# Optimization experiments

Hardware: AMD Instinct MI355X
Metric: run time of the kernel (lower is better)

Reference implementation:

```python
import jax, jax.numpy as jnp
from jax import lax
import numpy as np

N_LOOP, N_LAYER, FS = 2, 10, 2
RES_CH, DIL_CH, SKIP_CH, COND_DIM = 64, 128, 128, 80
DILATIONS = [2 ** i for i in range(N_LAYER)] * N_LOOP  # 20 layers
L = len(DILATIONS)
B, T = 4, 8192


def setup_inputs() -> dict:
    key = jax.random.key(0)
    ks = jax.random.split(key, 10)
    s = 0.05
    return {
        "x": jax.random.normal(ks[0], (B, RES_CH, T, 1), jnp.float32),
        "condition": jax.random.normal(ks[1], (B, COND_DIM, T, 1), jnp.float32),
        # stacked per-layer params (L layers)
        "conv_w": jax.random.normal(ks[2], (L, DIL_CH, RES_CH, FS), jnp.float32) * s,
        "conv_b": jax.random.normal(ks[3], (L, DIL_CH), jnp.float32) * s,
        "cond_w": jax.random.normal(ks[4], (L, DIL_CH, COND_DIM), jnp.float32) * s,
        "cond_b": jax.random.normal(ks[5], (L, DIL_CH), jnp.float32) * s,
        "res_w": jax.random.normal(ks[6], (L, RES_CH, DIL_CH // 2), jnp.float32) * s,
        "res_b": jax.random.normal(ks[7], (L, RES_CH), jnp.float32) * s,
        "skip_w": jax.random.normal(ks[8], (L, SKIP_CH, DIL_CH // 2), jnp.float32) * s,
        "skip_b": jax.random.normal(ks[9], (L, SKIP_CH), jnp.float32) * s,
    }


def reference(x, condition, conv_w, conv_b, cond_w, cond_b, res_w, res_b, skip_w, skip_b):
    # Drop trailing width-1 dim: [B,C,T,1] -> [B,C,T]
    xs = x[..., 0]
    cond = condition[..., 0]
    skip_total = None
    for i, d in enumerate(DILATIONS):
        # torch pads d*(FS-1) on both sides then crops [:T] == left-only causal pad
        h = lax.conv_general_dilated(
            xs, conv_w[i], window_strides=(1,),
            padding=[(d * (FS - 1), 0)], rhs_dilation=(d,),
            dimension_numbers=("NCH", "OIH", "NCH"),
        ) + conv_b[i][None, :, None]
        # 1x1 condition projection, broadcast add
        h = h + jnp.einsum("ch,bht->bct", cond_w[i], cond) + cond_b[i][None, :, None]
        tanh_z, sig_z = jnp.split(h, 2, axis=1)
        z = jnp.tanh(tanh_z) * jax.nn.sigmoid(sig_z)  # [B, DIL_CH//2, T]
        xs = jnp.einsum("oc,bct->bot", res_w[i], z) + res_b[i][None, :, None] + xs
        skip = jnp.einsum("oc,bct->bot", skip_w[i], z) + skip_b[i][None, :, None]
        skip_total = skip if skip_total is None else skip_total + skip
    return skip_total[..., None]  # [B, SKIP_CH, T, 1]
```

## Files before the change

kernel.cpp:

```cpp
#include <hip/hip_runtime.h>

#define BATCH 4
#define TLEN 8192
#define NLAYER 20
#define NTILE 128
#define GUARD 8
#define ATILE (NTILE + GUARD)
#define CELL 4096

typedef __attribute__((ext_vector_type(8))) short bf16x8;
typedef __attribute__((ext_vector_type(8))) unsigned short u16x8;
typedef __attribute__((ext_vector_type(4))) short s16x4;
typedef __attribute__((ext_vector_type(4))) float f32x4;

__device__ __forceinline__ unsigned short f2b(float f) {
    unsigned u = __float_as_uint(f);
    return (unsigned short)((u + 0x7fffu + ((u >> 16) & 1u)) >> 16);
}

__global__ void prep_w(const float* __restrict__ conv_w, const float* __restrict__ conv_b,
                       const float* __restrict__ cond_w, const float* __restrict__ cond_b,
                       const float* __restrict__ res_w,  const float* __restrict__ res_b,
                       const float* __restrict__ skip_w, const float* __restrict__ skip_b,
                       unsigned short* __restrict__ w1f, unsigned short* __restrict__ w2f,
                       unsigned short* __restrict__ wsf,
                       float* __restrict__ hb, float* __restrict__ rb, float* __restrict__ sbt) {
    const int l = blockIdx.x, tid = threadIdx.x;
    const int start = blockIdx.y * 256 + tid;
    for (int idx = start; idx < 7 * 8 * 512; idx += 2048) {
        int ks = idx >> 12;
        int lane = (idx >> 3) & 63, j = idx & 7, mf = (idx >> 9) & 7;
        int m = mf * 16 + (lane & 15);
        int k = ks * 32 + ((lane >> 4) << 3) + j;
        float v;
        if (k < 64)       v = conv_w[(((size_t)l * 128 + m) * 64 + k) * 2 + 0];
        else if (k < 128) v = conv_w[(((size_t)l * 128 + m) * 64 + (k - 64)) * 2 + 1];
        else if (k < 208) v = cond_w[((size_t)l * 128 + m) * 80 + (k - 128)];
        else              v = 0.0f;
        w1f[(size_t)l * 7 * 8 * 512 + idx] = f2b(v);
    }
    for (int idx = start; idx < 2 * 4 * 512; idx += 2048) {
        int ks = idx >> 11;
        int slot = (idx >> 9) & 3, lane = (idx >> 3) & 63, j = idx & 7;
        int m = slot * 16 + (lane & 15);
        int k = ks * 32 + ((lane >> 4) << 3) + j;
        w2f[(size_t)l * 2 * 4 * 512 + idx] = f2b(res_w[((size_t)l * 64 + m) * 64 + k]);
    }
    for (int idx = start; idx < 2 * 8 * 512; idx += 2048) {
        int ks = idx >> 12;
        int slot = (idx >> 9) & 7, lane = (idx >> 3) & 63, j = idx & 7;
        int m = slot * 16 + (lane & 15);
        int k = ks * 32 + ((lane >> 4) << 3) + j;
        wsf[(size_t)l * 2 * 8 * 512 + idx] = f2b(skip_w[((size_t)l * 128 + m) * 64 + k]);
    }
    if (blockIdx.y == 0) {
        if (tid < 128) hb[l * 128 + tid] = conv_b[l * 128 + tid] + cond_b[l * 128 + tid];
        if (tid < 64)  rb[l * 64 + tid] = res_b[l * 64 + tid];
        if (l == 0 && tid < 128) {
            float s = 0.f;
            for (int q = 0; q < NLAYER; ++q) s += skip_b[q * 128 + tid];
            sbt[tid] = s;
        }
    }
}

__global__ void prep_cond(const float* __restrict__ cond, unsigned short* __restrict__ condc) {
    __shared__ float ct[80][64];
    const int tile = blockIdx.x, b = blockIdx.y, tid = threadIdx.x;
    for (int idx = tid; idx < 80 * 64; idx += 256) {
        int ch = idx >> 6, n = idx & 63;
        ct[ch][n] = cond[((size_t)b * 80 + ch) * TLEN + tile * 64 + n];
    }
    __syncthreads();
    for (int idx = tid; idx < 12 * 64; idx += 256) {
        int cg = idx >> 6, n = idx & 63;
        u16x8 cell;
        #pragma unroll
        for (int j = 0; j < 8; ++j) {
            int ch = cg * 8 + j;
            cell[j] = (ch < 80) ? f2b(ct[ch][n]) : (unsigned short)0;
        }
        *(u16x8*)(condc + (((size_t)(b * NTILE + tile) * 12 + cg) * 64 + n) * 8) = cell;
    }
}

__global__ void prep_x(const float* __restrict__ x, unsigned short* __restrict__ xall,
                       unsigned* __restrict__ flags) {
    const int tile = blockIdx.x, b = blockIdx.y, tid = threadIdx.x;
    if (tile < GUARD) {
        s16x4 zh = {0, 0, 0, 0};
        for (int s = 0; s < NLAYER; ++s) {
            unsigned short* g = xall + ((size_t)s * BATCH + b) * ATILE * CELL + (size_t)tile * CELL;
            for (int idx = tid * 4; idx < CELL; idx += 1024)
                *(s16x4*)(g + idx) = zh;
        }
        if (tile == 0)
            for (int i = tid; i < NTILE * 32; i += 256)
                flags[(size_t)b * NTILE * 32 + i] = 0u;
        return;
    }
    __shared__ float xt[64][64];
    const int rt = tile - GUARD;
    for (int idx = tid; idx < 64 * 64; idx += 256) {
        int ch = idx >> 6, n = idx & 63;
        xt[ch][n] = x[((size_t)b * 64 + ch) * TLEN + rt * 64 + n];
    }
    __syncthreads();
    unsigned short* s0 = xall + ((size_t)b * ATILE + tile) * CELL;
    for (int idx = tid; idx < 8 * 64; idx += 256) {
        int cg = idx >> 6, n = idx & 63;
        unsigned short* dbf = s0 + ((size_t)cg * 64 + n) * 8;
        #pragma unroll
        for (int j = 0; j < 8; ++j) dbf[j] = f2b(xt[cg * 8 + j][n]);
    }
}

__global__ __launch_bounds__(256, 2) void wavenet_fused(
    const float* __restrict__ x, const unsigned short* __restrict__ condc,
    unsigned short* __restrict__ xall,
    const unsigned short* __restrict__ w1f, const unsigned short* __restrict__ w2f,
    const unsigned short* __restrict__ wsf,
    const float* __restrict__ hb, const float* __restrict__ rb,
    const float* __restrict__ sbt, float* __restrict__ out,
    unsigned* __restrict__ flags) {
    __shared__ unsigned short s_cond[12 * 512];
    __shared__ unsigned short s_xc[CELL];
    __shared__ unsigned short s_zc[CELL];
    __shared__ float H[128][67];

    const int b = blockIdx.y, tile = blockIdx.x, t0 = tile * 64;
    const int tid = threadIdx.x, lane = tid & 63;
    const int wv = __builtin_amdgcn_readfirstlane(tid >> 6);
    const int ln = lane & 15, lg = lane >> 4;
    const int r0 = wv * 16 + lg * 4;
    const size_t bslot = (size_t)BATCH * ATILE * CELL;

    {
        const u16x8* cc = (const u16x8*)(condc + (size_t)(b * NTILE + tile) * 12 * 512);
        u16x8* sc = (u16x8*)s_cond;
        for (int i = tid; i < 768; i += 256) sc[i] = cc[i];
        const u16x8* xc = (const u16x8*)(xall + ((size_t)b * ATILE + tile + GUARD) * CELL);
        u16x8* sx = (u16x8*)s_xc;
        for (int i = tid; i < 512; i += 256) sx[i] = xc[i];
    }

    f32x4 xsr[4];
    #pragma unroll
    for (int nf = 0; nf < 4; ++nf)
        #pragma unroll
        for (int r = 0; r < 4; ++r)
            xsr[nf][r] = x[((size_t)b * 64 + r0 + r) * TLEN + t0 + nf * 16 + ln];

    f32x4 skacc[2][4];
    #pragma unroll
    for (int mf = 0; mf < 2; ++mf)
        #pragma unroll
        for (int nf = 0; nf < 4; ++nf) skacc[mf][nf] = (f32x4){0.f, 0.f, 0.f, 0.f};

    __syncthreads();

    for (int l = 0; l < NLAYER; ++l) {
        const int dil = 1 << ((l < 10) ? l : (l - 10));

        if (l > 0) {
            if (tid == 0) {
                int tp = tile - ((dil + 63) >> 6);
                if (tp >= 0) {
                    const unsigned* fp = flags + ((size_t)b * NTILE + tp) * 32;
                    while (__hip_atomic_load(fp, __ATOMIC_RELAXED, __HIP_MEMORY_SCOPE_AGENT) < (unsigned)l)
                        __builtin_amdgcn_s_sleep(2);
                }
            }
            __syncthreads();
        }

        const unsigned short* xrb = xall + (size_t)l * bslot + (size_t)b * ATILE * CELL;

        f32x4 acc[2][4];
        #pragma unroll
        for (int mf = 0; mf < 2; ++mf)
            #pragma unroll
            for (int nf = 0; nf < 4; ++nf) acc[mf][nf] = (f32x4){0.f, 0.f, 0.f, 0.f};

        const unsigned short* w1l = w1f + (size_t)l * 7 * 8 * 512;
        #pragma unroll
        for (int ks = 0; ks < 7; ++ks) {
            bf16x8 af0 = *(const bf16x8*)(w1l + (size_t)(ks * 8 + wv * 2 + 0) * 512 + lane * 8);
            bf16x8 af1 = *(const bf16x8*)(w1l + (size_t)(ks * 8 + wv * 2 + 1) * 512 + lane * 8);
            bf16x8 bfr[4];
            if (ks < 2) {
                const int cg = ks * 4 + lg;
                #pragma unroll
                for (int nf = 0; nf < 4; ++nf) {
                    int u = t0 + nf * 16 + ln - dil + GUARD * 64;
                    bfr[nf] = *(const bf16x8*)(xrb + (((size_t)(u >> 6) * 8 + cg) * 64 + (u & 63)) * 8);
                }
            } else if (ks < 4) {
                const int cg = (ks - 2) * 4 + lg;
                #pragma unroll
                for (int nf = 0; nf < 4; ++nf)
                    bfr[nf] = *(const bf16x8*)(s_xc + ((cg * 64) + nf * 16 + ln) * 8);
            } else {
                const int cg = (ks - 4) * 4 + lg;
                #pragma unroll
                for (int nf = 0; nf < 4; ++nf)
                    bfr[nf] = *(const bf16x8*)(s_cond + ((cg * 64) + nf * 16 + ln) * 8);
            }
            #pragma unroll
            for (int mf = 0; mf < 2; ++mf)
                #pragma unroll
                for (int nf = 0; nf < 4; ++nf)
                    acc[mf][nf] = __builtin_amdgcn_mfma_f32_16x16x32_bf16(
                        (mf == 0) ? af0 : af1, bfr[nf], acc[mf][nf], 0, 0, 0);
        }

        const float* hbl = hb + l * 128;
        #pragma unroll
        for (int mf = 0; mf < 2; ++mf)
            #pragma unroll
            for (int nf = 0; nf < 4; ++nf)
                #pragma unroll
                for (int r = 0; r < 4; ++r) {
                    int m = wv * 32 + mf * 16 + lg * 4 + r;
                    H[m][nf * 16 + ln] = acc[mf][nf][r] + hbl[m];
                }
        __syncthreads();

        {
            const int n = tid & 63, g0 = (tid >> 6) * 16;
            #pragma unroll
            for (int half = 0; half < 2; ++half) {
                const int rbase = g0 + half * 8;
                u16x8 cell;
                #pragma unroll
                for (int i = 0; i < 4; ++i) {
                    int r = rbase + 2 * i;
                    float a0 = H[r][n],     b0 = H[r + 64][n];
                    float a1 = H[r + 1][n], b1 = H[r + 65][n];
                    float e0 = __expf(2.0f * a0), e1 = __expf(2.0f * a1);
                    float z0 = __fdividef(e0 - 1.0f, e0 + 1.0f) *
                               __fdividef(1.0f, 1.0f + __expf(-b0));
                    float z1 = __fdividef(e1 - 1.0f, e1 + 1.0f) *
                               __fdividef(1.0f, 1.0f + __expf(-b1));
                    cell[2 * i]     = f2b(z0);
                    cell[2 * i + 1] = f2b(z1);
                }
                *(u16x8*)(&s_zc[((rbase >> 3) * 64 + n) * 8]) = cell;
            }
        }
        __syncthreads();

        f32x4 acc2[4];
        #pragma unroll
        for (int nf = 0; nf < 4; ++nf) acc2[nf] = (f32x4){0.f, 0.f, 0.f, 0.f};
        const unsigned short* w2l = w2f + (size_t)l * 2 * 4 * 512;
        const unsigned short* wsl = wsf + (size_t)l * 2 * 8 * 512;
        #pragma unroll
        for (int ks = 0; ks < 2; ++ks) {
            bf16x8 bz[4];
            #pragma unroll
            for (int nf = 0; nf < 4; ++nf)
                bz[nf] = *(const bf16x8*)(&s_zc[(((ks * 4 + lg) * 64) + nf * 16 + ln) * 8]);
            bf16x8 a2 = *(const bf16x8*)(w2l + (size_t)(ks * 4 + wv) * 512 + lane * 8);
            bf16x8 s0 = *(const bf16x8*)(wsl + (size_t)(ks * 8 + wv * 2 + 0) * 512 + lane * 8);
            bf16x8 s1 = *(const bf16x8*)(wsl + (size_t)(ks * 8 + wv * 2 + 1) * 512 + lane * 8);
            #pragma unroll
            for (int nf = 0; nf < 4; ++nf) {
                acc2[nf]     = __builtin_amdgcn_mfma_f32_16x16x32_bf16(a2, bz[nf], acc2[nf], 0, 0, 0);
                skacc[0][nf] = __builtin_amdgcn_mfma_f32_16x16x32_bf16(s0, bz[nf], skacc[0][nf], 0, 0, 0);
                skacc[1][nf] = __builtin_amdgcn_mfma_f32_16x16x32_bf16(s1, bz[nf], skacc[1][nf], 0, 0, 0);
            }
        }

        {
            const float* rbl = rb + l * 64;
            const float bb0 = rbl[r0], bb1 = rbl[r0 + 1], bb2 = rbl[r0 + 2], bb3 = rbl[r0 + 3];
            const int cg = r0 >> 3, j0 = r0 & 7;
            unsigned short* xwt = xall + (size_t)(l + 1) * bslot +
                                  ((size_t)b * ATILE + tile + GUARD) * CELL;
            #pragma unroll
            for (int nf = 0; nf < 4; ++nf) {
                xsr[nf][0] += acc2[nf][0] + bb0;
                xsr[nf][1] += acc2[nf][1] + bb1;
                xsr[nf][2] += acc2[nf][2] + bb2;
                xsr[nf][3] += acc2[nf][3] + bb3;
                if (l < NLAYER - 1) {
                    int n = nf * 16 + ln;
                    union { s16x4 v; unsigned long long u; } pk;
                    pk.v.x = (short)f2b(xsr[nf][0]); pk.v.y = (short)f2b(xsr[nf][1]);
                    pk.v.z = (short)f2b(xsr[nf][2]); pk.v.w = (short)f2b(xsr[nf][3]);
                    *(s16x4*)(&s_xc[(cg * 64 + n) * 8 + j0]) = pk.v;
                    __hip_atomic_store((unsigned long long*)(xwt + ((size_t)cg * 64 + n) * 8 + j0),
                                       pk.u, __ATOMIC_RELAXED, __HIP_MEMORY_SCOPE_AGENT);
                }
            }
        }

        if (l < NLAYER - 1) {
            asm volatile("s_waitcnt vmcnt(0)" ::: "memory");
            __syncthreads();
            if (tid == 0)
                __hip_atomic_store(flags + ((size_t)b * NTILE + tile) * 32, (unsigned)(l + 1),
                                   __ATOMIC_RELAXED, __HIP_MEMORY_SCOPE_AGENT);
        }
    }

    #pragma unroll
    for (int mf = 0; mf < 2; ++mf)
        #pragma unroll
        for (int nf = 0; nf < 4; ++nf)
            #pragma unroll
            for (int r = 0; r < 4; ++r) {
                int m = wv * 32 + mf * 16 + lg * 4 + r;
                out[((size_t)b * 128 + m) * TLEN + t0 + nf * 16 + ln] =
                    skacc[mf][nf][r] + sbt[m];
            }
}

extern "C" void kernel_launch(void* const* d_in, const int* in_sizes, int n_in,
                              void* d_out, int out_size, void* d_ws, size_t ws_size,
                              hipStream_t stream) {
    const float* x      = (const float*)d_in[0];
    const float* cond   = (const float*)d_in[1];
    const float* conv_w = (const float*)d_in[2];
    const float* conv_b = (const float*)d_in[3];
    const float* cond_w = (const float*)d_in[4];
    const float* cond_b = (const float*)d_in[5];
    const float* res_w  = (const float*)d_in[6];
    const float* res_b  = (const float*)d_in[7];
    const float* skip_w = (const float*)d_in[8];
    const float* skip_b = (const float*)d_in[9];
    float* out = (float*)d_out;

    char* ws = (char*)d_ws;
    const size_t XALL  = (size_t)NLAYER * BATCH * ATILE * CELL * 2;
    const size_t COND  = (size_t)BATCH * NTILE * 12 * 512 * 2;
    const size_t W1    = (size_t)NLAYER * 7 * 8 * 512 * 2;
    const size_t W2    = (size_t)NLAYER * 2 * 4 * 512 * 2;
    const size_t WSF   = (size_t)NLAYER * 2 * 8 * 512 * 2;
    const size_t HB    = NLAYER * 128 * 4;
    const size_t RB    = NLAYER * 64 * 4;
    const size_t SBT   = 256 * 4;
    const size_t FLAGS = (size_t)BATCH * NTILE * 32 * 4;

    size_t off = 0;
    unsigned short* xall  = (unsigned short*)(ws + off); off += XALL;
    unsigned short* condc = (unsigned short*)(ws + off); off += COND;
    unsigned short* w1f   = (unsigned short*)(ws + off); off += W1;
    unsigned short* w2f   = (unsigned short*)(ws + off); off += W2;
    unsigned short* wsf   = (unsigned short*)(ws + off); off += WSF;
    float* hb  = (float*)(ws + off); off += HB;
    float* rb  = (float*)(ws + off); off += RB;
    float* sbt = (float*)(ws + off); off += SBT;
    unsigned* flags = (unsigned*)(ws + off); off += FLAGS;

    prep_w<<<dim3(NLAYER, 8), 256, 0, stream>>>(conv_w, conv_b, cond_w, cond_b,
                                                res_w, res_b, skip_w, skip_b,
                                                w1f, w2f, wsf, hb, rb, sbt);
    prep_cond<<<dim3(NTILE, BATCH), 256, 0, stream>>>(cond, condc);
    prep_x<<<dim3(ATILE, BATCH), 256, 0, stream>>>(x, xall, flags);

    wavenet_fused<<<dim3(NTILE, BATCH), 256, 0, stream>>>(
        x, condc, xall, w1f, w2f, wsf, hb, rb, sbt, out, flags);
}
```

Before: 145.7 us.

## Gate in registers, defer skip MFMAs past flag publish, merge prep kernels

Reorders the first-layer weight rows so each wave holds matching tanh and sigmoid rows, which lets the gated activation run directly on MFMA accumulators. This removes the fp32 H shared-memory round trip and one barrier per layer. The skip-projection MFMAs now run after the residual state is written and the flag is published, so the layer-to-layer dependency chain across tiles gets shorter. It also merges the x and condition prep kernels into one launch and uses the hardware packed bf16 convert. In exchange, the bz fragments are kept live longer, which raises register pressure.

```diff
diff --git a/kernel.cpp b/kernel.cpp
--- a/kernel.cpp
+++ b/kernel.cpp
@@ -16,6 +16,12 @@
 __device__ __forceinline__ unsigned short f2b(float f) {
     unsigned u = __float_as_uint(f);
     return (unsigned short)((u + 0x7fffu + ((u >> 16) & 1u)) >> 16);
+}
+
+__device__ __forceinline__ unsigned cvtpk(float lo, float hi) {
+    unsigned r;
+    asm("v_cvt_pk_bf16_f32 %0, %1, %2" : "=v"(r) : "v"(lo), "v"(hi));
+    return r;
 }
 
 __global__ void prep_w(const float* __restrict__ conv_w, const float* __restrict__ conv_b,
@@ -29,8 +35,8 @@
     const int start = blockIdx.y * 256 + tid;
     for (int idx = start; idx < 7 * 8 * 512; idx += 2048) {
         int ks = idx >> 12;
-        int lane = (idx >> 3) & 63, j = idx & 7, mf = (idx >> 9) & 7;
-        int m = mf * 16 + (lane & 15);
+        int slot = (idx >> 9) & 7, lane = (idx >> 3) & 63, j = idx & 7;
+        int m = (slot & 1) * 64 + (slot >> 1) * 16 + (lane & 15);
         int k = ks * 32 + ((lane >> 4) << 3) + j;
         float v;
         if (k < 64)       v = conv_w[(((size_t)l * 128 + m) * 64 + k) * 2 + 0];
@@ -64,28 +70,9 @@
     }
 }
 
-__global__ void prep_cond(const float* __restrict__ cond, unsigned short* __restrict__ condc) {
-    __shared__ float ct[80][64];
-    const int tile = blockIdx.x, b = blockIdx.y, tid = threadIdx.x;
-    for (int idx = tid; idx < 80 * 64; idx += 256) {
-        int ch = idx >> 6, n = idx & 63;
-        ct[ch][n] = cond[((size_t)b * 80 + ch) * TLEN + tile * 64 + n];
-    }
-    __syncthreads();
-    for (int idx = tid; idx < 12 * 64; idx += 256) {
-        int cg = idx >> 6, n = idx & 63;
-        u16x8 cell;
-        #pragma unroll
-        for (int j = 0; j < 8; ++j) {
-            int ch = cg * 8 + j;
-            cell[j] = (ch < 80) ? f2b(ct[ch][n]) : (unsigned short)0;
-        }
-        *(u16x8*)(condc + (((size_t)(b * NTILE + tile) * 12 + cg) * 64 + n) * 8) = cell;
-    }
-}
-
-__global__ void prep_x(const float* __restrict__ x, unsigned short* __restrict__ xall,
-                       unsigned* __restrict__ flags) {
+__global__ void prep_xc(const float* __restrict__ x, const float* __restrict__ cond,
+                        unsigned short* __restrict__ xall, unsigned short* __restrict__ condc,
+                        unsigned* __restrict__ flags) {
     const int tile = blockIdx.x, b = blockIdx.y, tid = threadIdx.x;
     if (tile < GUARD) {
         s16x4 zh = {0, 0, 0, 0};
@@ -100,10 +87,15 @@
         return;
     }
     __shared__ float xt[64][64];
+    __shared__ float ct[80][64];
     const int rt = tile - GUARD;
     for (int idx = tid; idx < 64 * 64; idx += 256) {
         int ch = idx >> 6, n = idx & 63;
         xt[ch][n] = x[((size_t)b * 64 + ch) * TLEN + rt * 64 + n];
+    }
+    for (int idx = tid; idx < 80 * 64; idx += 256) {
+        int ch = idx >> 6, n = idx & 63;
+        ct[ch][n] = cond[((size_t)b * 80 + ch) * TLEN + rt * 64 + n];
     }
     __syncthreads();
     unsigned short* s0 = xall + ((size_t)b * ATILE + tile) * CELL;
@@ -112,6 +104,16 @@
         unsigned short* dbf = s0 + ((size_t)cg * 64 + n) * 8;
         #pragma unroll
         for (int j = 0; j < 8; ++j) dbf[j] = f2b(xt[cg * 8 + j][n]);
+    }
+    for (int idx = tid; idx < 12 * 64; idx += 256) {
+        int cg = idx >> 6, n = idx & 63;
+        u16x8 cell;
+        #pragma unroll
+        for (int j = 0; j < 8; ++j) {
+            int ch = cg * 8 + j;
+            cell[j] = (ch < 80) ? f2b(ct[ch][n]) : (unsigned short)0;
+        }
+        *(u16x8*)(condc + (((size_t)(b * NTILE + rt) * 12 + cg) * 64 + n) * 8) = cell;
     }
 }
 
@@ -126,13 +128,13 @@
     __shared__ unsigned short s_cond[12 * 512];
     __shared__ unsigned short s_xc[CELL];
     __shared__ unsigned short s_zc[CELL];
-    __shared__ float H[128][67];
 
     const int b = blockIdx.y, tile = blockIdx.x, t0 = tile * 64;
     const int tid = threadIdx.x, lane = tid & 63;
     const int wv = __builtin_amdgcn_readfirstlane(tid >> 6);
     const int ln = lane & 15, lg = lane >> 4;
     const int r0 = wv * 16 + lg * 4;
+    const int cgz = r0 >> 3, j0z = r0 & 7;
     const size_t bslot = (size_t)BATCH * ATILE * CELL;
 
     {
@@ -178,9 +180,9 @@
 
         f32x4 acc[2][4];
         #pragma unroll
-        for (int mf = 0; mf < 2; ++mf)
-            #pragma unroll
-            for (int nf = 0; nf < 4; ++nf) acc[mf][nf] = (f32x4){0.f, 0.f, 0.f, 0.f};
+        for (int hf = 0; hf < 2; ++hf)
+            #pragma unroll
+            for (int nf = 0; nf < 4; ++nf) acc[hf][nf] = (f32x4){0.f, 0.f, 0.f, 0.f};
 
         const unsigned short* w1l = w1f + (size_t)l * 7 * 8 * 512;
         #pragma unroll
@@ -207,91 +209,74 @@
                     bfr[nf] = *(const bf16x8*)(s_cond + ((cg * 64) + nf * 16 + ln) * 8);
             }
             #pragma unroll
-            for (int mf = 0; mf < 2; ++mf)
+            for (int hf = 0; hf < 2; ++hf)
                 #pragma unroll
                 for (int nf = 0; nf < 4; ++nf)
-                    acc[mf][nf] = __builtin_amdgcn_mfma_f32_16x16x32_bf16(
-                        (mf == 0) ? af0 : af1, bfr[nf], acc[mf][nf], 0, 0, 0);
-        }
-
-        const float* hbl = hb + l * 128;
-        #pragma unroll
-        for (int mf = 0; mf < 2; ++mf)
+                    acc[hf][nf] = __builtin_amdgcn_mfma_f32_16x16x32_bf16(
+                        (hf == 0) ? af0 : af1, bfr[nf], acc[hf][nf], 0, 0, 0);
+        }
+
+        {
+            const float* hbl = hb + l * 128;
+            float4 hbt = *(const float4*)(hbl + r0);
+            float4 hbs = *(const float4*)(hbl + 64 + r0);
+            #pragma unroll
+            for (int nf = 0; nf < 4; ++nf) {
+                float zr[4];
+                #pragma unroll
+                for (int r = 0; r < 4; ++r) {
+                    float a  = acc[0][nf][r] + ((r == 0) ? hbt.x : (r == 1) ? hbt.y : (r == 2) ? hbt.z : hbt.w);
+                    float bs = acc[1][nf][r] + ((r == 0) ? hbs.x : (r == 1) ? hbs.y : (r == 2) ? hbs.z : hbs.w);
+                    float e = __expf(a + a);
+                    float s = __expf(-bs);
+                    zr[r] = __fdividef(e - 1.0f, (e + 1.0f) * (1.0f + s));
+                }
+                union { unsigned u32[2]; s16x4 v; } pk;
+                pk.u32[0] = cvtpk(zr[0], zr[1]);
+                pk.u32[1] = cvtpk(zr[2], zr[3]);
+                *(s16x4*)(&s_zc[((cgz * 64) + nf * 16 + ln) * 8 + j0z]) = pk.v;
+            }
+        }
+        __syncthreads();
+
+        bf16x8 bz[2][4];
+        #pragma unroll
+        for (int ks = 0; ks < 2; ++ks)
             #pragma unroll
             for (int nf = 0; nf < 4; ++nf)
-                #pragma unroll
-                for (int r = 0; r < 4; ++r) {
-                    int m = wv * 32 + mf * 16 + lg * 4 + r;
-                    H[m][nf * 16 + ln] = acc[mf][nf][r] + hbl[m];
-                }
-        __syncthreads();
-
-        {
-            const int n = tid & 63, g0 = (tid >> 6) * 16;
-            #pragma unroll
-            for (int half = 0; half < 2; ++half) {
-                const int rbase = g0 + half * 8;
-                u16x8 cell;
-                #pragma unroll
-                for (int i = 0; i < 4; ++i) {
-                    int r = rbase + 2 * i;
-                    float a0 = H[r][n],     b0 = H[r + 64][n];
-                    float a1 = H[r + 1][n], b1 = H[r + 65][n];
-                    float e0 = __expf(2.0f * a0), e1 = __expf(2.0f * a1);
-                    float z0 = __fdividef(e0 - 1.0f, e0 + 1.0f) *
-                               __fdividef(1.0f, 1.0f + __expf(-b0));
-                    float z1 = __fdividef(e1 - 1.0f, e1 + 1.0f) *
-                               __fdividef(1.0f, 1.0f + __expf(-b1));
-                    cell[2 * i]     = f2b(z0);
-                    cell[2 * i + 1] = f2b(z1);
-                }
-                *(u16x8*)(&s_zc[((rbase >> 3) * 64 + n) * 8]) = cell;
-            }
-        }
-        __syncthreads();
+                bz[ks][nf] = *(const bf16x8*)(&s_zc[(((ks * 4 + lg) * 64) + nf * 16 + ln) * 8]);
 
         f32x4 acc2[4];
         #pragma unroll
         for (int nf = 0; nf < 4; ++nf) acc2[nf] = (f32x4){0.f, 0.f, 0.f, 0.f};
         const unsigned short* w2l = w2f + (size_t)l * 2 * 4 * 512;
-        const unsigned short* wsl = wsf + (size_t)l * 2 * 8 * 512;
         #pragma unroll
         for (int ks = 0; ks < 2; ++ks) {
-            bf16x8 bz[4];
+            bf16x8 a2 = *(const bf16x8*)(w2l + (size_t)(ks * 4 + wv) * 512 + lane * 8);
             #pragma unroll
             for (int nf = 0; nf < 4; ++nf)
-                bz[nf] = *(const bf16x8*)(&s_zc[(((ks * 4 + lg) * 64) + nf * 16 + ln) * 8]);
-            bf16x8 a2 = *(const bf16x8*)(w2l + (size_t)(ks * 4 + wv) * 512 + lane * 8);
-            bf16x8 s0 = *(const bf16x8*)(wsl + (size_t)(ks * 8 + wv * 2 + 0) * 512 + lane * 8);
-            bf16x8 s1 = *(const bf16x8*)(wsl + (size_t)(ks * 8 + wv * 2 + 1) * 512 + lane * 8);
-            #pragma unroll
-            for (int nf = 0; nf < 4; ++nf) {
-                acc2[nf]     = __builtin_amdgcn_mfma_f32_16x16x32_bf16(a2, bz[nf], acc2[nf], 0, 0, 0);
-                skacc[0][nf] = __builtin_amdgcn_mfma_f32_16x16x32_bf16(s0, bz[nf], skacc[0][nf], 0, 0, 0);
-                skacc[1][nf] = __builtin_amdgcn_mfma_f32_16x16x32_bf16(s1, bz[nf], skacc[1][nf], 0, 0, 0);
-            }
+                acc2[nf] = __builtin_amdgcn_mfma_f32_16x16x32_bf16(a2, bz[ks][nf], acc2[nf], 0, 0, 0);
         }
 
         {
             const float* rbl = rb + l * 64;
-            const float bb0 = rbl[r0], bb1 = rbl[r0 + 1], bb2 = rbl[r0 + 2], bb3 = rbl[r0 + 3];
-            const int cg = r0 >> 3, j0 = r0 & 7;
+            float4 rbv = *(const float4*)(rbl + r0);
             unsigned short* xwt = xall + (size_t)(l + 1) * bslot +
                                   ((size_t)b * ATILE + tile + GUARD) * CELL;
             #pragma unroll
             for (int nf = 0; nf < 4; ++nf) {
-                xsr[nf][0] += acc2[nf][0] + bb0;
-                xsr[nf][1] += acc2[nf][1] + bb1;
-                xsr[nf][2] += acc2[nf][2] + bb2;
-                xsr[nf][3] += acc2[nf][3] + bb3;
+                xsr[nf][0] += acc2[nf][0] + rbv.x;
+                xsr[nf][1] += acc2[nf][1] + rbv.y;
+                xsr[nf][2] += acc2[nf][2] + rbv.z;
+                xsr[nf][3] += acc2[nf][3] + rbv.w;
                 if (l < NLAYER - 1) {
                     int n = nf * 16 + ln;
-                    union { s16x4 v; unsigned long long u; } pk;
-                    pk.v.x = (short)f2b(xsr[nf][0]); pk.v.y = (short)f2b(xsr[nf][1]);
-                    pk.v.z = (short)f2b(xsr[nf][2]); pk.v.w = (short)f2b(xsr[nf][3]);
-                    *(s16x4*)(&s_xc[(cg * 64 + n) * 8 + j0]) = pk.v;
-                    __hip_atomic_store((unsigned long long*)(xwt + ((size_t)cg * 64 + n) * 8 + j0),
-                                       pk.u, __ATOMIC_RELAXED, __HIP_MEMORY_SCOPE_AGENT);
+                    union { unsigned u32[2]; s16x4 v; unsigned long long u64; } pk;
+                    pk.u32[0] = cvtpk(xsr[nf][0], xsr[nf][1]);
+                    pk.u32[1] = cvtpk(xsr[nf][2], xsr[nf][3]);
+                    *(s16x4*)(&s_xc[(cgz * 64 + n) * 8 + j0z]) = pk.v;
+                    __hip_atomic_store((unsigned long long*)(xwt + ((size_t)cgz * 64 + n) * 8 + j0z),
+                                       pk.u64, __ATOMIC_RELAXED, __HIP_MEMORY_SCOPE_AGENT);
                 }
             }
         }
@@ -302,6 +287,18 @@
             if (tid == 0)
                 __hip_atomic_store(flags + ((size_t)b * NTILE + tile) * 32, (unsigned)(l + 1),
                                    __ATOMIC_RELAXED, __HIP_MEMORY_SCOPE_AGENT);
+        }
+
+        const unsigned short* wsl = wsf + (size_t)l * 2 * 8 * 512;
+        #pragma unroll
+        for (int ks = 0; ks < 2; ++ks) {
+            bf16x8 s0 = *(const bf16x8*)(wsl + (size_t)(ks * 8 + wv * 2 + 0) * 512 + lane * 8);
+            bf16x8 s1 = *(const bf16x8*)(wsl + (size_t)(ks * 8 + wv * 2 + 1) * 512 + lane * 8);
+            #pragma unroll
+            for (int nf = 0; nf < 4; ++nf) {
+                skacc[0][nf] = __builtin_amdgcn_mfma_f32_16x16x32_bf16(s0, bz[ks][nf], skacc[0][nf], 0, 0, 0);
+                skacc[1][nf] = __builtin_amdgcn_mfma_f32_16x16x32_bf16(s1, bz[ks][nf], skacc[1][nf], 0, 0, 0);
+            }
         }
     }
 
@@ -357,8 +354,7 @@
     prep_w<<<dim3(NLAYER, 8), 256, 0, stream>>>(conv_w, conv_b, cond_w, cond_b,
                                                 res_w, res_b, skip_w, skip_b,
                                                 w1f, w2f, wsf, hb, rb, sbt);
-    prep_cond<<<dim3(NTILE, BATCH), 256, 0, stream>>>(cond, condc);
-    prep_x<<<dim3(ATILE, BATCH), 256, 0, stream>>>(x, xall, flags);
+    prep_xc<<<dim3(ATILE, BATCH), 256, 0, stream>>>(x, cond, xall, condc, flags);
 
     wavenet_fused<<<dim3(NTILE, BATCH), 256, 0, stream>>>(
         x, condc, xall, w1f, w2f, wsf, hb, rb, sbt, out, flags);
```

Result: faster. 133.7 us (-8.2%).
